# Performance work log

Hardware: AMD Instinct MI355X
Metric: run time of the kernel (lower is better)

## Reference

```python
import jax, jax.numpy as jnp
import numpy as np

HIDDEN = 2048
N_HEADS = 16
HEAD_DIM = 128
ROPE_THETA = 10000.0
B = 8
S = 1024  # equal-length packed sequences; T = B*S


def _apply_rope(q, k, positions, base):
    # q, k: [T, H, D]; positions: [T] int. LLaMA rotate-half (non-interleaved) RoPE.
    D = q.shape[-1]
    inv_freq = 1.0 / (base ** (jnp.arange(0, D, 2, dtype=jnp.float32) / D))  # [D/2]
    ang = positions.astype(jnp.float32)[:, None] * inv_freq                  # [T, D/2]
    cos = jnp.cos(ang)[:, None, :]  # [T, 1, D/2]
    sin = jnp.sin(ang)[:, None, :]

    def rot(t):
        t1, t2 = jnp.split(t, 2, axis=-1)
        return jnp.concatenate([t1 * cos - t2 * sin, t1 * sin + t2 * cos], axis=-1)

    return rot(q), rot(k)


def setup_inputs() -> dict:
    key = jax.random.key(0)
    ks = jax.random.split(key, 6)
    T = B * S
    std = 1.0 / np.sqrt(HIDDEN)
    x = jax.random.normal(ks[0], (T, HIDDEN), dtype=jnp.float32)
    wq = jax.random.normal(ks[1], (HIDDEN, HIDDEN), dtype=jnp.float32) * std
    wk = jax.random.normal(ks[2], (HIDDEN, HIDDEN), dtype=jnp.float32) * std
    wv = jax.random.normal(ks[3], (HIDDEN, HIDDEN), dtype=jnp.float32) * std
    wo = jax.random.normal(ks[4], (HIDDEN, HIDDEN), dtype=jnp.float32) * std
    cu_seqlens = (jnp.arange(B + 1, dtype=jnp.int32) * S)
    context_lens = jax.random.randint(ks[5], (B,), 0, 512, dtype=jnp.int32)
    return {"x": x, "cu_seqlens": cu_seqlens, "context_lens": context_lens,
            "wq": wq, "wk": wk, "wv": wv, "wo": wo}


def reference(x, cu_seqlens, context_lens, wq, wk, wv, wo):
    # Prefill path: packed causal attention over B equal-length sequences.
    T = x.shape[0]
    H, D = N_HEADS, HEAD_DIM
    scale = 1.0 / np.sqrt(D)

    q = (x @ wq).reshape(T, H, D)
    k = (x @ wk).reshape(T, H, D)
    v = (x @ wv).reshape(T, H, D)

    # packed positions: per-seq arange offset by cache context lens
    positions = (context_lens.astype(jnp.int64)[:, None]
                 + jnp.arange(S, dtype=jnp.int64)[None, :]).reshape(T)
    q, k = _apply_rope(q, k, positions, ROPE_THETA)

    # block-diagonal causal attention: reshape packed -> [B, S, H, D]
    qb = q.reshape(B, S, H, D)
    kb = k.reshape(B, S, H, D)
    vb = v.reshape(B, S, H, D)
    scores = jnp.einsum('bqhd,bkhd->bhqk', qb, kb) * scale  # [B,H,S,S]
    causal = jnp.tril(jnp.ones((S, S), dtype=bool))
    scores = jnp.where(causal[None, None], scores, jnp.finfo(scores.dtype).min)
    probs = jax.nn.softmax(scores, axis=-1)
    attn = jnp.einsum('bhqk,bkhd->bqhd', probs, vb).reshape(T, H * D)
    return attn @ wo
```

## Files before the change

### kernel.cpp

```cpp
#include <hip/hip_runtime.h>
#include <hip/hip_bf16.h>
#include <math.h>

#define T_TOK 8192
#define HID   2048
#define NH    16
#define HD    128
#define SEQ   1024
#define NB    8
#define QKVN  6144

typedef __bf16 bf16x8 __attribute__((ext_vector_type(8)));
typedef float  f32x4  __attribute__((ext_vector_type(4)));

__global__ void cast_x_kernel(const float* __restrict__ in,
                              __hip_bfloat16* __restrict__ out, int n) {
  int i = blockIdx.x * blockDim.x + threadIdx.x;
  int base = i * 8;
  if (base >= n) return;
  const float4* p = (const float4*)(in + base);
  float4 a = p[0], b = p[1];
  union { uint4 u; __hip_bfloat16 h[8]; } o;
  o.h[0] = __float2bfloat16(a.x); o.h[1] = __float2bfloat16(a.y);
  o.h[2] = __float2bfloat16(a.z); o.h[3] = __float2bfloat16(a.w);
  o.h[4] = __float2bfloat16(b.x); o.h[5] = __float2bfloat16(b.y);
  o.h[6] = __float2bfloat16(b.z); o.h[7] = __float2bfloat16(b.w);
  *(uint4*)(out + base) = o.u;
}

__global__ void transpose_cast_kernel(const float* __restrict__ src,
                                      __hip_bfloat16* __restrict__ dst) {
  __shared__ float tile[32][33];
  int n0 = blockIdx.x * 32, k0 = blockIdx.y * 32;
  int tx = threadIdx.x, ty = threadIdx.y;
  for (int j = 0; j < 32; j += 8)
    tile[ty + j][tx] = src[(size_t)(k0 + ty + j) * HID + n0 + tx];
  __syncthreads();
  for (int j = 0; j < 32; j += 8)
    dst[(size_t)(n0 + ty + j) * HID + k0 + tx] = __float2bfloat16(tile[tx][ty + j]);
}

template <bool OUT_BF16>
__global__ __launch_bounds__(256)
void gemm_bf16(const __hip_bfloat16* __restrict__ A,
               const __hip_bfloat16* __restrict__ Bt,
               void* __restrict__ C, int M, int N, int K) {
  __shared__ __hip_bfloat16 As[128 * 32];
  __shared__ __hip_bfloat16 Bs[128 * 32];
  const int tid = threadIdx.x;
  const int lane = tid & 63;
  const int wid = tid >> 6;
  const int wr = wid >> 1, wc = wid & 1;
  const int m0 = blockIdx.y * 128;
  const int n0 = blockIdx.x * 128;

  f32x4 acc[4][4] = {};

  for (int kt = 0; kt < K; kt += 32) {
#pragma unroll
    for (int p = 0; p < 2; ++p) {
      int c = p * 256 + tid;
      int row = c >> 2, col = (c & 3) * 8;
      *(uint4*)&As[row * 32 + col] =
          *(const uint4*)(A + (size_t)(m0 + row) * K + kt + col);
      *(uint4*)&Bs[row * 32 + col] =
          *(const uint4*)(Bt + (size_t)(n0 + row) * K + kt + col);
    }
    __syncthreads();

    bf16x8 af[4], bf[4];
#pragma unroll
    for (int m = 0; m < 4; ++m) {
      int row = wr * 64 + m * 16 + (lane & 15);
      af[m] = *(const bf16x8*)((const char*)As + row * 64 + (lane >> 4) * 16);
    }
#pragma unroll
    for (int n = 0; n < 4; ++n) {
      int row = wc * 64 + n * 16 + (lane & 15);
      bf[n] = *(const bf16x8*)((const char*)Bs + row * 64 + (lane >> 4) * 16);
    }
#pragma unroll
    for (int m = 0; m < 4; ++m)
#pragma unroll
      for (int n = 0; n < 4; ++n)
        acc[m][n] = __builtin_amdgcn_mfma_f32_16x16x32_bf16(af[m], bf[n], acc[m][n], 0, 0, 0);
    __syncthreads();
  }

#pragma unroll
  for (int m = 0; m < 4; ++m) {
    int row = m0 + wr * 64 + m * 16 + ((lane >> 4) << 2);
#pragma unroll
    for (int r = 0; r < 4; ++r) {
#pragma unroll
      for (int n = 0; n < 4; ++n) {
        int col = n0 + wc * 64 + n * 16 + (lane & 15);
        float v = acc[m][n][r];
        if (OUT_BF16)
          ((__hip_bfloat16*)C)[(size_t)(row + r) * N + col] = __float2bfloat16(v);
        else
          ((float*)C)[(size_t)(row + r) * N + col] = v;
      }
    }
  }
}

__global__ void rope_kernel(__hip_bfloat16* __restrict__ qkv,
                            const int* __restrict__ context_lens) {
  int idx = blockIdx.x * blockDim.x + threadIdx.x;
  if (idx >= T_TOK * NH * 64) return;
  int d2 = idx & 63;
  int h = (idx >> 6) & 15;
  int t = idx >> 10;
  int b = t >> 10;
  float pos = (float)(context_lens[b] + (t & 1023));
  float freq = expf((float)d2 * (-9.210340371976184f / 64.0f));
  float ang = pos * freq;
  float s, c;
  sincosf(ang, &s, &c);
  size_t base = (size_t)t * QKVN + h * HD + d2;
  float x1 = __bfloat162float(qkv[base]);
  float x2 = __bfloat162float(qkv[base + 64]);
  qkv[base]      = __float2bfloat16(x1 * c - x2 * s);
  qkv[base + 64] = __float2bfloat16(x1 * s + x2 * c);
  float y1 = __bfloat162float(qkv[base + HID]);
  float y2 = __bfloat162float(qkv[base + HID + 64]);
  qkv[base + HID]      = __float2bfloat16(y1 * c - y2 * s);
  qkv[base + HID + 64] = __float2bfloat16(y1 * s + y2 * c);
}

__global__ __launch_bounds__(256)
void attn_kernel(const __hip_bfloat16* __restrict__ qkv,
                 __hip_bfloat16* __restrict__ attn) {
  const int qt = blockIdx.x;
  const int h = blockIdx.y;
  const int b = blockIdx.z;
  const int tid = threadIdx.x, lane = tid & 63, wid = tid >> 6;
  const int q0 = qt * 64;
  const size_t seq_base = (size_t)b * SEQ;

  __shared__ __hip_bfloat16 Ks[32][136];
  __shared__ __hip_bfloat16 Vt[128][40];
  __shared__ __hip_bfloat16 Pl[4][16][40];

  bf16x8 qf[4];
  {
    int t = q0 + wid * 16 + (lane & 15);
    const __hip_bfloat16* qp = qkv + (seq_base + t) * QKVN + h * HD + (lane >> 4) * 8;
#pragma unroll
    for (int kc = 0; kc < 4; ++kc) qf[kc] = *(const bf16x8*)(qp + kc * 32);
  }

  f32x4 acc_o[8] = {};
  float mrow[4] = {-INFINITY, -INFINITY, -INFINITY, -INFINITY};
  float lrow[4] = {0.f, 0.f, 0.f, 0.f};
  const float scale = 0.08838834764831845f;

  const int ntiles = (q0 + 64) / 32;
  for (int kt = 0; kt < ntiles; ++kt) {
    const int kv0 = kt * 32;
    __syncthreads();
#pragma unroll
    for (int j = 0; j < 2; ++j) {
      int c = j * 256 + tid;
      int row = c >> 4, col = (c & 15) * 8;
      const __hip_bfloat16* kp = qkv + (seq_base + kv0 + row) * QKVN + HID + h * HD + col;
      *(uint4*)&Ks[row][col] = *(const uint4*)kp;
      const __hip_bfloat16* vp = qkv + (seq_base + kv0 + row) * QKVN + 2 * HID + h * HD + col;
      uint4 vd = *(const uint4*)vp;
      const ushort* vs = (const ushort*)&vd;
#pragma unroll
      for (int i = 0; i < 8; ++i) *(ushort*)&Vt[col + i][row] = vs[i];
    }
    __syncthreads();

    f32x4 s[2];
#pragma unroll
    for (int ct = 0; ct < 2; ++ct) {
      f32x4 a = {};
      int row = ct * 16 + (lane & 15);
#pragma unroll
      for (int kc = 0; kc < 4; ++kc) {
        bf16x8 kf = *(const bf16x8*)((const char*)&Ks[0][0] + row * 272 + kc * 64 + (lane >> 4) * 16);
        a = __builtin_amdgcn_mfma_f32_16x16x32_bf16(qf[kc], kf, a, 0, 0, 0);
      }
      s[ct] = a;
    }

    int qrow_base = q0 + wid * 16 + (lane >> 4) * 4;
#pragma unroll
    for (int ct = 0; ct < 2; ++ct) {
      int kvcol = kv0 + ct * 16 + (lane & 15);
#pragma unroll
      for (int r = 0; r < 4; ++r) {
        float v = s[ct][r] * scale;
        s[ct][r] = (kvcol > qrow_base + r) ? -INFINITY : v;
      }
    }

    float corr[4];
#pragma unroll
    for (int r = 0; r < 4; ++r) {
      float t = fmaxf(s[0][r], s[1][r]);
      t = fmaxf(t, __shfl_xor(t, 1));
      t = fmaxf(t, __shfl_xor(t, 2));
      t = fmaxf(t, __shfl_xor(t, 4));
      t = fmaxf(t, __shfl_xor(t, 8));
      float mnew = fmaxf(mrow[r], t);
      corr[r] = __expf(mrow[r] - mnew);
      float p0 = __expf(s[0][r] - mnew);
      float p1 = __expf(s[1][r] - mnew);
      float sum = p0 + p1;
      sum += __shfl_xor(sum, 1);
      sum += __shfl_xor(sum, 2);
      sum += __shfl_xor(sum, 4);
      sum += __shfl_xor(sum, 8);
      lrow[r] = lrow[r] * corr[r] + sum;
      mrow[r] = mnew;
      int prow = (lane >> 4) * 4 + r;
      Pl[wid][prow][0 * 16 + (lane & 15)] = __float2bfloat16(p0);
      Pl[wid][prow][1 * 16 + (lane & 15)] = __float2bfloat16(p1);
    }

#pragma unroll
    for (int n = 0; n < 8; ++n)
#pragma unroll
      for (int r = 0; r < 4; ++r) acc_o[n][r] *= corr[r];

    bf16x8 pa = *(const bf16x8*)((const char*)&Pl[wid][0][0] + (lane & 15) * 80 + (lane >> 4) * 16);
#pragma unroll
    for (int n = 0; n < 8; ++n) {
      bf16x8 vf = *(const bf16x8*)((const char*)&Vt[0][0] + (n * 16 + (lane & 15)) * 80 + (lane >> 4) * 16);
      acc_o[n] = __builtin_amdgcn_mfma_f32_16x16x32_bf16(pa, vf, acc_o[n], 0, 0, 0);
    }
  }

#pragma unroll
  for (int n = 0; n < 8; ++n)
#pragma unroll
    for (int r = 0; r < 4; ++r) {
      int qrow = q0 + wid * 16 + (lane >> 4) * 4 + r;
      float v = acc_o[n][r] / lrow[r];
      attn[(seq_base + qrow) * HID + h * HD + n * 16 + (lane & 15)] = __float2bfloat16(v);
    }
}

extern "C" void kernel_launch(void* const* d_in, const int* in_sizes, int n_in,
                              void* d_out, int out_size, void* d_ws, size_t ws_size,
                              hipStream_t stream) {
  const float* x  = (const float*)d_in[0];
  const int* ctx  = (const int*)d_in[2];
  const float* wq = (const float*)d_in[3];
  const float* wk = (const float*)d_in[4];
  const float* wv = (const float*)d_in[5];
  const float* wo = (const float*)d_in[6];

  char* ws = (char*)d_ws;
  __hip_bfloat16* xbf   = (__hip_bfloat16*)(ws);
  __hip_bfloat16* wqkvT = (__hip_bfloat16*)(ws + 33554432);
  __hip_bfloat16* woT   = (__hip_bfloat16*)(ws + 58720256);
  __hip_bfloat16* qkv   = (__hip_bfloat16*)(ws + 67108864);
  __hip_bfloat16* attn  = (__hip_bfloat16*)(ws);

  cast_x_kernel<<<T_TOK * HID / 8 / 256, 256, 0, stream>>>(x, xbf, T_TOK * HID);

  dim3 tb(32, 8), tg(HID / 32, HID / 32);
  transpose_cast_kernel<<<tg, tb, 0, stream>>>(wq, wqkvT);
  transpose_cast_kernel<<<tg, tb, 0, stream>>>(wk, wqkvT + (size_t)HID * HID);
  transpose_cast_kernel<<<tg, tb, 0, stream>>>(wv, wqkvT + (size_t)2 * HID * HID);
  transpose_cast_kernel<<<tg, tb, 0, stream>>>(wo, woT);

  gemm_bf16<true><<<dim3(QKVN / 128, T_TOK / 128), 256, 0, stream>>>(
      xbf, wqkvT, qkv, T_TOK, QKVN, HID);

  rope_kernel<<<T_TOK * NH * 64 / 256, 256, 0, stream>>>(qkv, ctx);

  attn_kernel<<<dim3(SEQ / 64, NH, NB), 256, 0, stream>>>(qkv, attn);

  gemm_bf16<false><<<dim3(HID / 128, T_TOK / 128), 256, 0, stream>>>(
      attn, woT, (void*)d_out, T_TOK, HID, HID);
}
```

Baseline: 991.0 us.

## Use direct global-to-LDS GEMM loads, pre-transpose V, write attention output in place

The GEMM tile loads now use global_load_lds 16-byte transfers that write straight into shared memory instead of passing through registers. A new kernel pre-transposes V per batch and head into a separate buffer, so the attention kernel can fill its V tile with vector loads instead of eight scalar transposed LDS stores per lane. The attention output overwrites the Q slot of the qkv buffer, and the output GEMM reads it through a new leading-dimension argument. This adds an extra launch and a round trip of V through global memory, and relies on the direct-to-LDS loads being complete before the barrier.

```diff
diff --git a/kernel.cpp b/kernel.cpp
--- a/kernel.cpp
+++ b/kernel.cpp
@@ -12,6 +12,12 @@
 
 typedef __bf16 bf16x8 __attribute__((ext_vector_type(8)));
 typedef float  f32x4  __attribute__((ext_vector_type(4)));
+
+__device__ __forceinline__ void gload_lds16(const void* g, void* l) {
+  __builtin_amdgcn_global_load_lds(
+      (const __attribute__((address_space(1))) void*)g,
+      (__attribute__((address_space(3))) void*)l, 16, 0, 0);
+}
 
 __global__ void cast_x_kernel(const float* __restrict__ in,
                               __hip_bfloat16* __restrict__ out, int n) {
@@ -40,11 +46,26 @@
     dst[(size_t)(n0 + ty + j) * HID + k0 + tx] = __float2bfloat16(tile[tx][ty + j]);
 }
 
+__global__ void vtrans_kernel(const __hip_bfloat16* __restrict__ qkv,
+                              __hip_bfloat16* __restrict__ vt) {
+  __shared__ __hip_bfloat16 tile[32][33];
+  const int s0 = blockIdx.x * 32;
+  const int d0 = blockIdx.y * 32;
+  const int bh = blockIdx.z;
+  const int b = bh >> 4, h = bh & 15;
+  const int tx = threadIdx.x, ty = threadIdx.y;
+  for (int j = 0; j < 32; j += 8)
+    tile[ty + j][tx] = qkv[(size_t)(b * SEQ + s0 + ty + j) * QKVN + 2 * HID + h * HD + d0 + tx];
+  __syncthreads();
+  for (int j = 0; j < 32; j += 8)
+    vt[(size_t)(bh * HD + d0 + ty + j) * SEQ + s0 + tx] = tile[tx][ty + j];
+}
+
 template <bool OUT_BF16>
 __global__ __launch_bounds__(256)
 void gemm_bf16(const __hip_bfloat16* __restrict__ A,
                const __hip_bfloat16* __restrict__ Bt,
-               void* __restrict__ C, int M, int N, int K) {
+               void* __restrict__ C, int M, int N, int K, int lda) {
   __shared__ __hip_bfloat16 As[128 * 32];
   __shared__ __hip_bfloat16 Bs[128 * 32];
   const int tid = threadIdx.x;
@@ -58,13 +79,13 @@
 
   for (int kt = 0; kt < K; kt += 32) {
 #pragma unroll
-    for (int p = 0; p < 2; ++p) {
-      int c = p * 256 + tid;
-      int row = c >> 2, col = (c & 3) * 8;
-      *(uint4*)&As[row * 32 + col] =
-          *(const uint4*)(A + (size_t)(m0 + row) * K + kt + col);
-      *(uint4*)&Bs[row * 32 + col] =
-          *(const uint4*)(Bt + (size_t)(n0 + row) * K + kt + col);
+    for (int j = 0; j < 2; ++j) {
+      int cw = j * 256 + wid * 64;
+      int c = cw + lane;
+      gload_lds16(A + (size_t)(m0 + (c >> 2)) * lda + kt + (c & 3) * 8,
+                  (char*)As + cw * 16);
+      gload_lds16(Bt + (size_t)(n0 + (c >> 2)) * K + kt + (c & 3) * 8,
+                  (char*)Bs + cw * 16);
     }
     __syncthreads();
 
@@ -130,17 +151,18 @@
 }
 
 __global__ __launch_bounds__(256)
-void attn_kernel(const __hip_bfloat16* __restrict__ qkv,
-                 __hip_bfloat16* __restrict__ attn) {
+void attn_kernel(__hip_bfloat16* __restrict__ qkv,
+                 const __hip_bfloat16* __restrict__ vt) {
   const int qt = blockIdx.x;
   const int h = blockIdx.y;
   const int b = blockIdx.z;
+  const int bh = b * NH + h;
   const int tid = threadIdx.x, lane = tid & 63, wid = tid >> 6;
   const int q0 = qt * 64;
   const size_t seq_base = (size_t)b * SEQ;
 
   __shared__ __hip_bfloat16 Ks[32][136];
-  __shared__ __hip_bfloat16 Vt[128][40];
+  __shared__ __hip_bfloat16 Vts[128][40];
   __shared__ __hip_bfloat16 Pl[4][16][40];
 
   bf16x8 qf[4];
@@ -163,14 +185,12 @@
 #pragma unroll
     for (int j = 0; j < 2; ++j) {
       int c = j * 256 + tid;
-      int row = c >> 4, col = (c & 15) * 8;
-      const __hip_bfloat16* kp = qkv + (seq_base + kv0 + row) * QKVN + HID + h * HD + col;
-      *(uint4*)&Ks[row][col] = *(const uint4*)kp;
-      const __hip_bfloat16* vp = qkv + (seq_base + kv0 + row) * QKVN + 2 * HID + h * HD + col;
-      uint4 vd = *(const uint4*)vp;
-      const ushort* vs = (const ushort*)&vd;
-#pragma unroll
-      for (int i = 0; i < 8; ++i) *(ushort*)&Vt[col + i][row] = vs[i];
+      int krow = c >> 4, kcol = (c & 15) * 8;
+      *(uint4*)&Ks[krow][kcol] = *(const uint4*)(
+          qkv + (seq_base + kv0 + krow) * QKVN + HID + h * HD + kcol);
+      int vrow = c >> 2, vseg = (c & 3) * 8;
+      *(uint4*)&Vts[vrow][vseg] = *(const uint4*)(
+          vt + (size_t)(bh * HD + vrow) * SEQ + kv0 + vseg);
     }
     __syncthreads();
 
@@ -230,7 +250,7 @@
     bf16x8 pa = *(const bf16x8*)((const char*)&Pl[wid][0][0] + (lane & 15) * 80 + (lane >> 4) * 16);
 #pragma unroll
     for (int n = 0; n < 8; ++n) {
-      bf16x8 vf = *(const bf16x8*)((const char*)&Vt[0][0] + (n * 16 + (lane & 15)) * 80 + (lane >> 4) * 16);
+      bf16x8 vf = *(const bf16x8*)((const char*)&Vts[0][0] + (n * 16 + (lane & 15)) * 80 + (lane >> 4) * 16);
       acc_o[n] = __builtin_amdgcn_mfma_f32_16x16x32_bf16(pa, vf, acc_o[n], 0, 0, 0);
     }
   }
@@ -241,7 +261,7 @@
     for (int r = 0; r < 4; ++r) {
       int qrow = q0 + wid * 16 + (lane >> 4) * 4 + r;
       float v = acc_o[n][r] / lrow[r];
-      attn[(seq_base + qrow) * HID + h * HD + n * 16 + (lane & 15)] = __float2bfloat16(v);
+      qkv[(seq_base + qrow) * QKVN + h * HD + n * 16 + (lane & 15)] = __float2bfloat16(v);
     }
 }
 
@@ -257,10 +277,10 @@
 
   char* ws = (char*)d_ws;
   __hip_bfloat16* xbf   = (__hip_bfloat16*)(ws);
+  __hip_bfloat16* vt    = (__hip_bfloat16*)(ws);
   __hip_bfloat16* wqkvT = (__hip_bfloat16*)(ws + 33554432);
   __hip_bfloat16* woT   = (__hip_bfloat16*)(ws + 58720256);
   __hip_bfloat16* qkv   = (__hip_bfloat16*)(ws + 67108864);
-  __hip_bfloat16* attn  = (__hip_bfloat16*)(ws);
 
   cast_x_kernel<<<T_TOK * HID / 8 / 256, 256, 0, stream>>>(x, xbf, T_TOK * HID);
 
@@ -271,12 +291,14 @@
   transpose_cast_kernel<<<tg, tb, 0, stream>>>(wo, woT);
 
   gemm_bf16<true><<<dim3(QKVN / 128, T_TOK / 128), 256, 0, stream>>>(
-      xbf, wqkvT, qkv, T_TOK, QKVN, HID);
+      xbf, wqkvT, qkv, T_TOK, QKVN, HID, HID);
 
   rope_kernel<<<T_TOK * NH * 64 / 256, 256, 0, stream>>>(qkv, ctx);
 
-  attn_kernel<<<dim3(SEQ / 64, NH, NB), 256, 0, stream>>>(qkv, attn);
+  vtrans_kernel<<<dim3(SEQ / 32, HD / 32, NB * NH), dim3(32, 8), 0, stream>>>(qkv, vt);
+
+  attn_kernel<<<dim3(SEQ / 64, NH, NB), 256, 0, stream>>>(qkv, vt);
 
   gemm_bf16<false><<<dim3(HID / 128, T_TOK / 128), 256, 0, stream>>>(
-      attn, woT, (void*)d_out, T_TOK, HID, HID);
-}
+      qkv, woT, (void*)d_out, T_TOK, HID, HID, QKVN);
+}
```

New measurement: 797.7 us. 19.5% less time.
